# Performance work log

Hardware: AMD Instinct MI355X
Metric: run time of the kernel (lower is better)

## Reference

```python
import jax, jax.numpy as jnp
import numpy as np

D_MODEL = 1024
N_HEADS = 16
D_K = 64
CHUNK_LEN = 64


def setup_inputs() -> dict:
    key = jax.random.key(0)
    ks = jax.random.split(key, 10)
    B, S = 4, 2048
    NC, NN, NL = 32, 2, 128
    s = 1.0 / np.sqrt(D_MODEL)
    inp = {
        "query": jax.random.normal(ks[0], (B, S, D_MODEL), dtype=jnp.float32),
        "key": jax.random.normal(ks[1], (B, NC, NN, NL, D_MODEL), dtype=jnp.float32),
        # Linear weights stored as [in, out] (equivalent to torch W.T)
        "Wq": jax.random.normal(ks[2], (D_MODEL, N_HEADS * D_K), dtype=jnp.float32) * s,
        "bq": jnp.zeros((N_HEADS * D_K,), dtype=jnp.float32),
        "Wk": jax.random.normal(ks[3], (D_MODEL, N_HEADS * D_K), dtype=jnp.float32) * s,
        "bk": jnp.zeros((N_HEADS * D_K,), dtype=jnp.float32),
        "Wv": jax.random.normal(ks[4], (D_MODEL, N_HEADS * D_K), dtype=jnp.float32) * s,
        "bv": jnp.zeros((N_HEADS * D_K,), dtype=jnp.float32),
        "Wo": jax.random.normal(ks[5], (N_HEADS * D_K, D_MODEL), dtype=jnp.float32) * s,
        "bo": jnp.zeros((D_MODEL,), dtype=jnp.float32),
    }
    return inp


def reference(query, key, Wq, bq, Wk, bk, Wv, bv, Wo, bo):
    B, S, D = query.shape
    _, NC, NN, NL, _ = key.shape
    L = NN * NL  # kv length per chunk
    # reshape query into chunks: [B, NC, chunk_len, D]
    q_in = query.reshape(B, NC, CHUNK_LEN, D)
    kv_in = key.reshape(B, NC, L, D)  # key used for both K and V in the original
    # projections, split heads: [B, NC, H, T, d_k]
    q = (q_in @ Wq + bq).reshape(B, NC, CHUNK_LEN, N_HEADS, D_K).transpose(0, 1, 3, 2, 4)
    k = (kv_in @ Wk + bk).reshape(B, NC, L, N_HEADS, D_K).transpose(0, 1, 3, 2, 4)
    v = (kv_in @ Wv + bv).reshape(B, NC, L, N_HEADS, D_K).transpose(0, 1, 3, 2, 4)
    # attention per (batch, chunk, head)
    scores = jnp.einsum("bchqd,bchkd->bchqk", q, k) / jnp.sqrt(jnp.float32(D_K))
    attn = jax.nn.softmax(scores, axis=-1)
    o = jnp.einsum("bchqk,bchkd->bchqd", attn, v)
    # merge heads: [B, NC, chunk_len, H*d_k]
    o = o.transpose(0, 1, 3, 2, 4).reshape(B, NC, CHUNK_LEN, N_HEADS * D_K)
    out = o @ Wo + bo
    return out.reshape(B, S, D)
```

## Files before the change

kernel.cpp:

```cpp
#include <hip/hip_runtime.h>
#include <hip/hip_bf16.h>
#include <stdint.h>

#define DMODEL 1024
#define NHEADS 16
#define DK 64
#define TQ 64
#define LKV 256
#define MQ 8192
#define MKV 32768

typedef __bf16 bf16x8 __attribute__((ext_vector_type(8)));
typedef float f32x4 __attribute__((ext_vector_type(4)));
typedef unsigned short u16x8 __attribute__((ext_vector_type(8)));
typedef unsigned short u16;

__device__ __forceinline__ unsigned short f2bf(float f) {
    union { float f; unsigned int i; } x; x.f = f;
    unsigned int r = (x.i + 0x7FFFu + ((x.i >> 16) & 1u)) >> 16;
    return (unsigned short)r;
}

__device__ __forceinline__ void gload_lds16(const void* g, void* l) {
    __builtin_amdgcn_global_load_lds(
        (const __attribute__((address_space(1))) unsigned int*)g,
        (__attribute__((address_space(3))) unsigned int*)l, 16, 0, 0);
}

__global__ __launch_bounds__(256) void cvt_f32_bf16(const float* __restrict__ in,
                                                    unsigned short* __restrict__ out) {
    long long i = ((long long)blockIdx.x * 256 + threadIdx.x) * 8;
    f32x4 a = *(const f32x4*)(in + i);
    f32x4 b = *(const f32x4*)(in + i + 4);
    u16x8 o;
    o[0] = f2bf(a[0]); o[1] = f2bf(a[1]); o[2] = f2bf(a[2]); o[3] = f2bf(a[3]);
    o[4] = f2bf(b[0]); o[5] = f2bf(b[1]); o[6] = f2bf(b[2]); o[7] = f2bf(b[3]);
    *(u16x8*)(out + i) = o;
}

__global__ __launch_bounds__(256) void transpose_w_cvt(const float* __restrict__ in,
                                                       unsigned short* __restrict__ out) {
    __shared__ float tile[64][65];
    int bi = blockIdx.y, bj = blockIdx.x;
    int tid = threadIdx.x;
    int c = tid & 63, r0 = tid >> 6;
#pragma unroll
    for (int p = 0; p < 16; ++p) {
        int r = r0 + 4 * p;
        tile[r][c] = in[(size_t)(bi * 64 + r) * 1024 + bj * 64 + c];
    }
    __syncthreads();
#pragma unroll
    for (int p = 0; p < 16; ++p) {
        int r = r0 + 4 * p;
        out[(size_t)(bj * 64 + r) * 1024 + bi * 64 + c] = f2bf(tile[c][r]);
    }
}


__device__ __forceinline__ void stageA64(const u16* src, u16* ldsTile, int row0, int tid) {
    int w = tid >> 6, l = tid & 63;
    int r = row0 + w * 8 + (l >> 3);
    int k16 = (l & 7) ^ ((l >> 3) & 7);
    gload_lds16(src + (size_t)r * 1024 + k16 * 8, ldsTile + (size_t)(row0 + w * 8) * 64);
}
__device__ __forceinline__ void stageB64(const u16* src, u16* ldsTile, int j, int odd, int tid) {
    int w = tid >> 6, l = tid & 63;
    int ib = j * 64 + w * 8;
    int rowbase = ((ib >> 5) << 6) + (ib & 31) + (odd ? 32 : 0);
    int r = rowbase + (l >> 3);
    int k16 = (l & 7) ^ ((l >> 3) & 7);
    gload_lds16(src + (size_t)r * 1024 + k16 * 8, ldsTile + (size_t)rowbase * 64);
}

#define VMWAIT2() asm volatile("s_waitcnt vmcnt(2)" ::: "memory")

template <int OUTMODE>
__global__ __launch_bounds__(512, 2) void gemm256(const u16* __restrict__ A,
                                                  const u16* __restrict__ Bt,
                                                  const float* __restrict__ bias,
                                                  void* __restrict__ OutV, int nBx) {
    __shared__ alignas(16) u16 lds[65536];
    u16* ldsA0 = lds;          u16* ldsA1 = lds + 16384;
    u16* ldsB0 = lds + 32768;  u16* ldsB1 = lds + 49152;

    int tid = threadIdx.x, lane = tid & 63, wid = tid >> 6;
    int wm = wid >> 2, wn = wid & 3;

    int nB = nBx * 4;
    int bid = blockIdx.x;
    int qq = nB >> 3, rr = nB & 7;
    int xcd = bid & 7, idx = bid >> 3;
    int wg = (xcd < rr) ? xcd * (qq + 1) + idx : rr * (qq + 1) + (xcd - rr) * qq + idx;
    int m0 = (wg >> 2) * 256;
    int n0 = (wg & 3) * 256;

    const u16* aSrc = A + (size_t)m0 * 1024;
    const u16* bSrc = Bt + (size_t)n0 * 1024;

    f32x4 zero = {0.f, 0.f, 0.f, 0.f};
    f32x4 acc[8][4];
#pragma unroll
    for (int i = 0; i < 8; ++i)
#pragma unroll
        for (int j = 0; j < 4; ++j) acc[i][j] = zero;

    stageA64(aSrc, ldsA0, 0, tid);   stageA64(aSrc, ldsA0, 128, tid);
    stageB64(bSrc, ldsB0, 0, 0, tid); stageB64(bSrc, ldsB0, 1, 0, tid);
    stageB64(bSrc, ldsB0, 0, 1, tid); stageB64(bSrc, ldsB0, 1, 1, tid);
    stageA64(aSrc, ldsA0, 64, tid);  stageA64(aSrc, ldsA0, 192, tid);
    asm volatile("s_waitcnt vmcnt(0)" ::: "memory");
    __builtin_amdgcn_s_barrier();
    asm volatile("" ::: "memory");

    for (int t = 0; t < 16; ++t) {
        int cur = t & 1;
        u16* lA = cur ? ldsA1 : ldsA0;
        u16* lB = cur ? ldsB1 : ldsB0;
        u16* pA = cur ? ldsA0 : ldsA1;
        u16* pB = cur ? ldsB0 : ldsB1;
        const u16* aNext = aSrc + (t + 1) * 64;
        const u16* bNext = bSrc + (t + 1) * 64;
        bool pf = (t < 15);

#pragma unroll
        for (int q = 0; q < 4; ++q) {
            if (q < 3) VMWAIT2();
            bf16x8 aF[4][2], bF[2][2];
            int mrow0 = wm * 128 + (q >> 1) * 64;
#pragma unroll
            for (int mf = 0; mf < 4; ++mf) {
                int row = mrow0 + mf * 16 + (lane & 15);
#pragma unroll
                for (int kk = 0; kk < 2; ++kk) {
                    int k16 = kk * 4 + (lane >> 4);
                    aF[mf][kk] = *(const bf16x8*)&lA[row * 64 + ((k16 ^ (row & 7)) << 3)];
                }
            }
            int nrow0 = wn * 64 + (q & 1) * 32;
#pragma unroll
            for (int nf = 0; nf < 2; ++nf) {
                int row = nrow0 + nf * 16 + (lane & 15);
#pragma unroll
                for (int kk = 0; kk < 2; ++kk) {
                    int k16 = kk * 4 + (lane >> 4);
                    bF[nf][kk] = *(const bf16x8*)&lB[row * 64 + ((k16 ^ (row & 7)) << 3)];
                }
            }
            if (pf) {
                if (q == 0)      { stageA64(aNext, pA, 0, tid);    stageA64(aNext, pA, 128, tid); }
                else if (q == 1) { stageB64(bNext, pB, 0, 0, tid); stageB64(bNext, pB, 1, 0, tid); }
                else if (q == 2) { stageB64(bNext, pB, 0, 1, tid); stageB64(bNext, pB, 1, 1, tid); }
                else             { stageA64(aNext, pA, 64, tid);   stageA64(aNext, pA, 192, tid); }
            }
            __builtin_amdgcn_s_barrier();
            asm volatile("" ::: "memory");
            __builtin_amdgcn_s_setprio(1);
#pragma unroll
            for (int mf = 0; mf < 4; ++mf)
#pragma unroll
                for (int nf = 0; nf < 2; ++nf)
#pragma unroll
                    for (int kk = 0; kk < 2; ++kk)
                        acc[(q >> 1) * 4 + mf][(q & 1) * 2 + nf] =
                            __builtin_amdgcn_mfma_f32_16x16x32_bf16(
                                aF[mf][kk], bF[nf][kk],
                                acc[(q >> 1) * 4 + mf][(q & 1) * 2 + nf], 0, 0, 0);
            __builtin_amdgcn_s_setprio(0);
            __builtin_amdgcn_s_barrier();
            asm volatile("" ::: "memory");
        }
    }

    float bv[4];
#pragma unroll
    for (int NF = 0; NF < 4; ++NF) bv[NF] = bias[n0 + wn * 64 + NF * 16 + (lane & 15)];

    if (OUTMODE == 0) {
        u16* Out = (u16*)OutV;
#pragma unroll
        for (int MF = 0; MF < 8; ++MF)
#pragma unroll
            for (int r = 0; r < 4; ++r) {
                size_t row = (size_t)(m0 + wm * 128 + MF * 16 + (lane >> 4) * 4 + r);
#pragma unroll
                for (int NF = 0; NF < 4; ++NF)
                    Out[row * 1024 + n0 + wn * 64 + NF * 16 + (lane & 15)] =
                        f2bf(acc[MF][NF][r] + bv[NF]);
            }
    } else if (OUTMODE == 1) {
        u16* Out = (u16*)OutV;
#pragma unroll
        for (int MF = 0; MF < 8; ++MF)
#pragma unroll
            for (int r = 0; r < 4; ++r) {
                int gm = m0 + wm * 128 + MF * 16 + (lane >> 4) * 4 + r;
                int bc2 = gm >> 8, lv = gm & 255;
#pragma unroll
                for (int NF = 0; NF < 4; ++NF) {
                    int n = n0 + wn * 64 + NF * 16 + (lane & 15);
                    int hh = n >> 6, dd = n & 63;
                    Out[(size_t)((bc2 * 16 + hh) * 64 + dd) * 256 + lv] =
                        f2bf(acc[MF][NF][r] + bv[NF]);
                }
            }
    } else {
        float* Out = (float*)OutV;
#pragma unroll
        for (int MF = 0; MF < 8; ++MF)
#pragma unroll
            for (int r = 0; r < 4; ++r) {
                size_t row = (size_t)(m0 + wm * 128 + MF * 16 + (lane >> 4) * 4 + r);
#pragma unroll
                for (int NF = 0; NF < 4; ++NF)
                    Out[row * 1024 + n0 + wn * 64 + NF * 16 + (lane & 15)] =
                        acc[MF][NF][r] + bv[NF];
            }
    }
}

__global__ __launch_bounds__(256) void attn_kernel(const unsigned short* __restrict__ Q,
                                                   const unsigned short* __restrict__ K,
                                                   const unsigned short* __restrict__ Vt,
                                                   unsigned short* O) {
    __shared__ alignas(16) unsigned short pLds[64 * 264];

    int tid = threadIdx.x;
    int lane = tid & 63, w = tid >> 6;
    int bc = blockIdx.x >> 4, h = blockIdx.x & 15;
    int fr = lane & 15, g = lane >> 4;

    const unsigned short* qb = Q + (size_t)(bc * 64 + w * 16 + fr) * 1024 + h * 64 + g * 8;
    bf16x8 qf0 = *(const bf16x8*)qb;
    bf16x8 qf1 = *(const bf16x8*)(qb + 32);

    const unsigned short* kb = K + (size_t)(bc * 256 + fr) * 1024 + h * 64 + g * 8;

    f32x4 zero = {0.f, 0.f, 0.f, 0.f};
    f32x4 sc[16];
#pragma unroll
    for (int nt = 0; nt < 16; ++nt) sc[nt] = zero;

#pragma unroll
    for (int nt = 0; nt < 16; ++nt) {
        bf16x8 kf0 = *(const bf16x8*)(kb + (size_t)(nt * 16) * 1024);
        bf16x8 kf1 = *(const bf16x8*)(kb + (size_t)(nt * 16) * 1024 + 32);
        sc[nt] = __builtin_amdgcn_mfma_f32_16x16x32_bf16(qf0, kf0, sc[nt], 0, 0, 0);
        sc[nt] = __builtin_amdgcn_mfma_f32_16x16x32_bf16(qf1, kf1, sc[nt], 0, 0, 0);
    }

    const float scale = 0.125f;
    float mx[4], sum[4];
#pragma unroll
    for (int r = 0; r < 4; ++r) {
        float m = -1e30f;
#pragma unroll
        for (int nt = 0; nt < 16; ++nt) {
            sc[nt][r] *= scale;
            m = fmaxf(m, sc[nt][r]);
        }
#pragma unroll
        for (int x = 1; x < 16; x <<= 1) m = fmaxf(m, __shfl_xor(m, x, 64));
        mx[r] = m;
        sum[r] = 0.f;
    }
#pragma unroll
    for (int nt = 0; nt < 16; ++nt)
#pragma unroll
        for (int r = 0; r < 4; ++r) {
            float p = __expf(sc[nt][r] - mx[r]);
            sum[r] += p;
            pLds[(w * 16 + g * 4 + r) * 264 + nt * 16 + fr] = f2bf(p);
        }
#pragma unroll
    for (int r = 0; r < 4; ++r)
#pragma unroll
        for (int x = 1; x < 16; x <<= 1) sum[r] += __shfl_xor(sum[r], x, 64);

    __syncthreads();

    f32x4 oa[4];
#pragma unroll
    for (int nt = 0; nt < 4; ++nt) oa[nt] = zero;

    const unsigned short* vtb = Vt + (size_t)((bc * 16 + h) * 64) * 256;
#pragma unroll
    for (int ks = 0; ks < 8; ++ks) {
        bf16x8 pf = *(const bf16x8*)&pLds[(w * 16 + fr) * 264 + ks * 32 + g * 8];
#pragma unroll
        for (int nt = 0; nt < 4; ++nt) {
            bf16x8 vf = *(const bf16x8*)(vtb + (size_t)(nt * 16 + fr) * 256 + ks * 32 + g * 8);
            oa[nt] = __builtin_amdgcn_mfma_f32_16x16x32_bf16(pf, vf, oa[nt], 0, 0, 0);
        }
    }

    float rs[4];
#pragma unroll
    for (int r = 0; r < 4; ++r) rs[r] = 1.0f / sum[r];

    unsigned short* ob = O + (size_t)(bc * 64 + w * 16 + g * 4) * 1024 + h * 64 + fr;
#pragma unroll
    for (int nt = 0; nt < 4; ++nt)
#pragma unroll
        for (int r = 0; r < 4; ++r)
            ob[(size_t)r * 1024 + nt * 16] = f2bf(oa[nt][r] * rs[r]);
}

extern "C" void kernel_launch(void* const* d_in, const int* in_sizes, int n_in,
                              void* d_out, int out_size, void* d_ws, size_t ws_size,
                              hipStream_t stream) {
    const float* query = (const float*)d_in[0];
    const float* keyin = (const float*)d_in[1];
    const float* Wq = (const float*)d_in[2];
    const float* bq = (const float*)d_in[3];
    const float* Wk = (const float*)d_in[4];
    const float* bk = (const float*)d_in[5];
    const float* Wv = (const float*)d_in[6];
    const float* bv = (const float*)d_in[7];
    const float* Wo = (const float*)d_in[8];
    const float* bo = (const float*)d_in[9];

    unsigned short* ws = (unsigned short*)d_ws;
    const size_t MB1 = 1024 * 1024;

    unsigned short* WqT = ws;
    unsigned short* WkT = ws + MB1;
    unsigned short* WvT = ws + 2 * MB1;
    unsigned short* WoT = ws + 3 * MB1;
    unsigned short* qb16 = ws + 4 * MB1;
    unsigned short* Qp   = qb16 + (size_t)MQ * 1024;
    unsigned short* kvb  = Qp + (size_t)MQ * 1024;

    size_t ws_elems = ws_size / 2;
    size_t fixed = 4 * MB1 + 2 * (size_t)MQ * 1024;
    size_t avail = (ws_elems > fixed) ? (ws_elems - fixed) : 0;
    long long max_rows = (long long)(avail / (3 * 1024));
    int slice_rows = (int)((max_rows / 256) * 256);
    if (slice_rows > MKV) slice_rows = MKV;
    if (slice_rows < 256) slice_rows = 256;

    unsigned short* Kp = kvb + (size_t)slice_rows * 1024;
    unsigned short* Vt = Kp + (size_t)slice_rows * 1024;

    dim3 tb(256);
    transpose_w_cvt<<<dim3(16, 16), tb, 0, stream>>>(Wq, WqT);
    transpose_w_cvt<<<dim3(16, 16), tb, 0, stream>>>(Wk, WkT);
    transpose_w_cvt<<<dim3(16, 16), tb, 0, stream>>>(Wv, WvT);
    transpose_w_cvt<<<dim3(16, 16), tb, 0, stream>>>(Wo, WoT);

    cvt_f32_bf16<<<dim3(MQ * 1024 / (256 * 8)), tb, 0, stream>>>(query, qb16);
    gemm256<0><<<dim3((MQ / 256) * 4), dim3(512), 0, stream>>>(qb16, WqT, bq, Qp, MQ / 256);

    for (int r0 = 0; r0 < MKV; r0 += slice_rows) {
        int rows = MKV - r0;
        if (rows > slice_rows) rows = slice_rows;
        cvt_f32_bf16<<<dim3(rows * 1024 / (256 * 8)), tb, 0, stream>>>(
            keyin + (size_t)r0 * 1024, kvb);
        gemm256<0><<<dim3((rows / 256) * 4), dim3(512), 0, stream>>>(kvb, WkT, bk, Kp, rows / 256);
        gemm256<1><<<dim3((rows / 256) * 4), dim3(512), 0, stream>>>(kvb, WvT, bv, Vt, rows / 256);
        size_t qoff = (size_t)(r0 / 4) * 1024;
        attn_kernel<<<dim3((rows / 256) * 16), tb, 0, stream>>>(
            Qp + qoff, Kp, Vt, Qp + qoff);
    }

    gemm256<2><<<dim3((MQ / 256) * 4), dim3(512), 0, stream>>>(Qp, WoT, bo, d_out, MQ / 256);
}
```

Measured before the change: 363.9 us.

## Reorder gemm256 fragment reuse and use smaller-tile GEMM for Q/O projections

The 256x256 GEMM main loop now keeps A and B fragments in registers across quarter-steps, serpentining through the (m,n) quadrants so each LDS fragment is read once per K-step instead of re-read per quarter. The Q and output projections (8192 rows) switch to a new simpler 128x128-tile kernel with a 2D grid, giving more blocks than the 128-block gemm256 launch on a many-CU GPU. The new kernel has no double buffering and a single sync per 32-wide K step, so its latency hiding is weaker. The register-held fragments also raise register pressure in gemm256.

```diff
diff --git a/kernel.cpp b/kernel.cpp
--- a/kernel.cpp
+++ b/kernel.cpp
@@ -57,6 +57,86 @@
     }
 }
 
+template <int OUTMODE>
+__global__ __launch_bounds__(256) void gemm_bias(const unsigned short* __restrict__ A,
+                                                 const unsigned short* __restrict__ Bt,
+                                                 const float* __restrict__ bias,
+                                                 void* __restrict__ OutV) {
+    __shared__ alignas(16) unsigned short aLds[128 * 32];
+    __shared__ alignas(16) unsigned short bLds[128 * 32];
+
+    int tid = threadIdx.x;
+    int lane = tid & 63, wid = tid >> 6;
+    int m0 = blockIdx.x * 128;
+    int n0 = blockIdx.y * 128;
+    int wr = (wid >> 1) * 64, wc = (wid & 1) * 64;
+
+    f32x4 zero = {0.f, 0.f, 0.f, 0.f};
+    f32x4 acc[4][4];
+#pragma unroll
+    for (int i = 0; i < 4; ++i)
+#pragma unroll
+        for (int j = 0; j < 4; ++j) acc[i][j] = zero;
+
+    int sr = lane >> 2;
+    int sk = (lane & 3) * 8;
+    const unsigned short* aG = A + (size_t)(m0 + sr) * 1024 + sk;
+    const unsigned short* bG = Bt + (size_t)(n0 + sr) * 1024 + sk;
+    int c0 = wid, c1 = wid + 4;
+
+    int fr = lane & 15, fg = (lane >> 4) * 8;
+
+    for (int kt = 0; kt < 1024; kt += 32) {
+        gload_lds16(aG + (size_t)(c0 * 16) * 1024 + kt, aLds + c0 * 512);
+        gload_lds16(aG + (size_t)(c1 * 16) * 1024 + kt, aLds + c1 * 512);
+        gload_lds16(bG + (size_t)(c0 * 16) * 1024 + kt, bLds + c0 * 512);
+        gload_lds16(bG + (size_t)(c1 * 16) * 1024 + kt, bLds + c1 * 512);
+        __syncthreads();
+
+        bf16x8 af[4], bf[4];
+#pragma unroll
+        for (int mt = 0; mt < 4; ++mt)
+            af[mt] = *(const bf16x8*)&aLds[(wr + mt * 16 + fr) * 32 + fg];
+#pragma unroll
+        for (int nt = 0; nt < 4; ++nt)
+            bf[nt] = *(const bf16x8*)&bLds[(wc + nt * 16 + fr) * 32 + fg];
+#pragma unroll
+        for (int mt = 0; mt < 4; ++mt)
+#pragma unroll
+            for (int nt = 0; nt < 4; ++nt)
+                acc[mt][nt] = __builtin_amdgcn_mfma_f32_16x16x32_bf16(af[mt], bf[nt], acc[mt][nt], 0, 0, 0);
+        __syncthreads();
+    }
+
+    float bv[4];
+#pragma unroll
+    for (int nt = 0; nt < 4; ++nt) bv[nt] = bias[n0 + wc + nt * 16 + fr];
+
+    if (OUTMODE == 0) {
+        unsigned short* Out = (unsigned short*)OutV;
+#pragma unroll
+        for (int mt = 0; mt < 4; ++mt)
+#pragma unroll
+            for (int r = 0; r < 4; ++r) {
+                size_t row = (size_t)(m0 + wr + mt * 16 + (lane >> 4) * 4 + r);
+#pragma unroll
+                for (int nt = 0; nt < 4; ++nt)
+                    Out[row * 1024 + n0 + wc + nt * 16 + fr] = f2bf(acc[mt][nt][r] + bv[nt]);
+            }
+    } else {
+        float* Out = (float*)OutV;
+#pragma unroll
+        for (int mt = 0; mt < 4; ++mt)
+#pragma unroll
+            for (int r = 0; r < 4; ++r) {
+                size_t row = (size_t)(m0 + wr + mt * 16 + (lane >> 4) * 4 + r);
+#pragma unroll
+                for (int nt = 0; nt < 4; ++nt)
+                    Out[row * 1024 + n0 + wc + nt * 16 + fr] = acc[mt][nt][r] + bv[nt];
+            }
+    }
+}
+
 
 __device__ __forceinline__ void stageA64(const u16* src, u16* ldsTile, int row0, int tid) {
     int w = tid >> 6, l = tid & 63;
@@ -74,6 +154,7 @@
 }
 
 #define VMWAIT2() asm volatile("s_waitcnt vmcnt(2)" ::: "memory")
+#define SBAR()    do { __builtin_amdgcn_s_barrier(); asm volatile("" ::: "memory"); } while (0)
 
 template <int OUTMODE>
 __global__ __launch_bounds__(512, 2) void gemm256(const u16* __restrict__ A,
@@ -105,13 +186,46 @@
 #pragma unroll
         for (int j = 0; j < 4; ++j) acc[i][j] = zero;
 
-    stageA64(aSrc, ldsA0, 0, tid);   stageA64(aSrc, ldsA0, 128, tid);
+    bf16x8 aR[4][2], b0R[2][2], b1R[2][2];
+
+#define READ_A(lA, half)                                                         \
+    do {                                                                         \
+        _Pragma("unroll") for (int mf = 0; mf < 4; ++mf) {                       \
+            int row = wm * 128 + (half) * 64 + mf * 16 + (lane & 15);            \
+            _Pragma("unroll") for (int kk = 0; kk < 2; ++kk) {                   \
+                int k16 = kk * 4 + (lane >> 4);                                  \
+                aR[mf][kk] = *(const bf16x8*)&(lA)[row * 64 + ((k16 ^ (row & 7)) << 3)]; \
+            }                                                                    \
+        }                                                                        \
+    } while (0)
+#define READ_B(lB, half, dst)                                                    \
+    do {                                                                         \
+        _Pragma("unroll") for (int nf = 0; nf < 2; ++nf) {                       \
+            int row = wn * 64 + (half) * 32 + nf * 16 + (lane & 15);             \
+            _Pragma("unroll") for (int kk = 0; kk < 2; ++kk) {                   \
+                int k16 = kk * 4 + (lane >> 4);                                  \
+                dst[nf][kk] = *(const bf16x8*)&(lB)[row * 64 + ((k16 ^ (row & 7)) << 3)]; \
+            }                                                                    \
+        }                                                                        \
+    } while (0)
+#define MFMA16(mh, nh, bR)                                                       \
+    do {                                                                         \
+        __builtin_amdgcn_s_setprio(1);                                           \
+        _Pragma("unroll") for (int mf = 0; mf < 4; ++mf)                         \
+            _Pragma("unroll") for (int nf = 0; nf < 2; ++nf)                     \
+                _Pragma("unroll") for (int kk = 0; kk < 2; ++kk)                 \
+                    acc[(mh)*4 + mf][(nh)*2 + nf] =                              \
+                        __builtin_amdgcn_mfma_f32_16x16x32_bf16(                 \
+                            aR[mf][kk], bR[nf][kk], acc[(mh)*4 + mf][(nh)*2 + nf], 0, 0, 0); \
+        __builtin_amdgcn_s_setprio(0);                                           \
+    } while (0)
+
+    stageA64(aSrc, ldsA0, 0, tid);    stageA64(aSrc, ldsA0, 128, tid);
     stageB64(bSrc, ldsB0, 0, 0, tid); stageB64(bSrc, ldsB0, 1, 0, tid);
     stageB64(bSrc, ldsB0, 0, 1, tid); stageB64(bSrc, ldsB0, 1, 1, tid);
-    stageA64(aSrc, ldsA0, 64, tid);  stageA64(aSrc, ldsA0, 192, tid);
+    stageA64(aSrc, ldsA0, 64, tid);   stageA64(aSrc, ldsA0, 192, tid);
     asm volatile("s_waitcnt vmcnt(0)" ::: "memory");
-    __builtin_amdgcn_s_barrier();
-    asm volatile("" ::: "memory");
+    SBAR();
 
     for (int t = 0; t < 16; ++t) {
         int cur = t & 1;
@@ -123,53 +237,32 @@
         const u16* bNext = bSrc + (t + 1) * 64;
         bool pf = (t < 15);
 
-#pragma unroll
-        for (int q = 0; q < 4; ++q) {
-            if (q < 3) VMWAIT2();
-            bf16x8 aF[4][2], bF[2][2];
-            int mrow0 = wm * 128 + (q >> 1) * 64;
-#pragma unroll
-            for (int mf = 0; mf < 4; ++mf) {
-                int row = mrow0 + mf * 16 + (lane & 15);
-#pragma unroll
-                for (int kk = 0; kk < 2; ++kk) {
-                    int k16 = kk * 4 + (lane >> 4);
-                    aF[mf][kk] = *(const bf16x8*)&lA[row * 64 + ((k16 ^ (row & 7)) << 3)];
-                }
-            }
-            int nrow0 = wn * 64 + (q & 1) * 32;
-#pragma unroll
-            for (int nf = 0; nf < 2; ++nf) {
-                int row = nrow0 + nf * 16 + (lane & 15);
-#pragma unroll
-                for (int kk = 0; kk < 2; ++kk) {
-                    int k16 = kk * 4 + (lane >> 4);
-                    bF[nf][kk] = *(const bf16x8*)&lB[row * 64 + ((k16 ^ (row & 7)) << 3)];
-                }
-            }
-            if (pf) {
-                if (q == 0)      { stageA64(aNext, pA, 0, tid);    stageA64(aNext, pA, 128, tid); }
-                else if (q == 1) { stageB64(bNext, pB, 0, 0, tid); stageB64(bNext, pB, 1, 0, tid); }
-                else if (q == 2) { stageB64(bNext, pB, 0, 1, tid); stageB64(bNext, pB, 1, 1, tid); }
-                else             { stageA64(aNext, pA, 64, tid);   stageA64(aNext, pA, 192, tid); }
-            }
-            __builtin_amdgcn_s_barrier();
-            asm volatile("" ::: "memory");
-            __builtin_amdgcn_s_setprio(1);
-#pragma unroll
-            for (int mf = 0; mf < 4; ++mf)
-#pragma unroll
-                for (int nf = 0; nf < 2; ++nf)
-#pragma unroll
-                    for (int kk = 0; kk < 2; ++kk)
-                        acc[(q >> 1) * 4 + mf][(q & 1) * 2 + nf] =
-                            __builtin_amdgcn_mfma_f32_16x16x32_bf16(
-                                aF[mf][kk], bF[nf][kk],
-                                acc[(q >> 1) * 4 + mf][(q & 1) * 2 + nf], 0, 0, 0);
-            __builtin_amdgcn_s_setprio(0);
-            __builtin_amdgcn_s_barrier();
-            asm volatile("" ::: "memory");
-        }
+        VMWAIT2();
+        READ_A(lA, 0);
+        READ_B(lB, 0, b0R);
+        if (pf) { stageA64(aNext, pA, 0, tid); stageA64(aNext, pA, 128, tid); }
+        SBAR();
+        MFMA16(0, 0, b0R);
+        SBAR();
+
+        VMWAIT2();
+        READ_B(lB, 1, b1R);
+        if (pf) { stageB64(bNext, pB, 0, 0, tid); stageB64(bNext, pB, 1, 0, tid); }
+        SBAR();
+        MFMA16(0, 1, b1R);
+        SBAR();
+
+        READ_A(lA, 1);
+        if (pf) { stageB64(bNext, pB, 0, 1, tid); stageB64(bNext, pB, 1, 1, tid); }
+        SBAR();
+        MFMA16(1, 1, b1R);
+        SBAR();
+
+        VMWAIT2();
+        if (pf) { stageA64(aNext, pA, 64, tid); stageA64(aNext, pA, 192, tid); }
+        SBAR();
+        MFMA16(1, 0, b0R);
+        SBAR();
     }
 
     float bv[4];
@@ -217,6 +310,9 @@
                         acc[MF][NF][r] + bv[NF];
             }
     }
+#undef READ_A
+#undef READ_B
+#undef MFMA16
 }
 
 __global__ __launch_bounds__(256) void attn_kernel(const unsigned short* __restrict__ Q,
@@ -349,7 +445,7 @@
     transpose_w_cvt<<<dim3(16, 16), tb, 0, stream>>>(Wo, WoT);
 
     cvt_f32_bf16<<<dim3(MQ * 1024 / (256 * 8)), tb, 0, stream>>>(query, qb16);
-    gemm256<0><<<dim3((MQ / 256) * 4), dim3(512), 0, stream>>>(qb16, WqT, bq, Qp, MQ / 256);
+    gemm_bias<0><<<dim3(MQ / 128, 8), tb, 0, stream>>>(qb16, WqT, bq, Qp);
 
     for (int r0 = 0; r0 < MKV; r0 += slice_rows) {
         int rows = MKV - r0;
@@ -363,5 +459,5 @@
             Qp + qoff, Kp, Vt, Qp + qoff);
     }
 
-    gemm256<2><<<dim3((MQ / 256) * 4), dim3(512), 0, stream>>>(Qp, WoT, bo, d_out, MQ / 256);
-}
+    gemm_bias<2><<<dim3(MQ / 128, 8), tb, 0, stream>>>(Qp, WoT, bo, d_out);
+}
```

New measurement: 328.6 us. 1.11x faster.
